# Optimization experiments

Hardware: AMD Instinct MI355X
Metric: run time of the kernel (lower is better)

The kernel has to match this reference:

```python
import jax, jax.numpy as jnp
import numpy as np

DIM = 1024
NUM_HEADS = 16
HEAD_DIM = DIM // NUM_HEADS


def apply_rotary_embed(x, thetas):
    # x: (..., seq, d), thetas: (seq, d) broadcast over leading dims
    x1, x2 = jnp.split(x, 2, axis=-1)
    x_rot = jnp.concatenate([-x2, x1], axis=-1)
    return x * jnp.cos(thetas) + x_rot * jnp.sin(thetas)


def setup_inputs() -> dict:
    key = jax.random.key(0)
    ks = jax.random.split(key, 8)
    B, Nx, Nc = 4, 1024, 2048
    x = jax.random.normal(ks[0], (B, Nx, DIM), dtype=jnp.float32)
    c = jax.random.normal(ks[1], (B, Nc, DIM), dtype=jnp.float32)
    x_pos_embed = jax.random.normal(ks[2], (Nx, HEAD_DIM), dtype=jnp.float32)
    c_pos_embed = jax.random.normal(ks[3], (Nc, HEAD_DIM), dtype=jnp.float32)
    s = 1.0 / np.sqrt(DIM)
    Wq = jax.random.normal(ks[4], (DIM, DIM), dtype=jnp.float32) * s
    Wkv = jax.random.normal(ks[5], (DIM, 2 * DIM), dtype=jnp.float32) * s
    Wproj = jax.random.normal(ks[6], (DIM, DIM), dtype=jnp.float32) * s
    bproj = jnp.zeros((DIM,), dtype=jnp.float32)
    return {"x": x, "c": c, "x_pos_embed": x_pos_embed, "c_pos_embed": c_pos_embed,
            "Wq": Wq, "Wkv": Wkv, "Wproj": Wproj, "bproj": bproj}


def reference(x, c, x_pos_embed, c_pos_embed, Wq, Wkv, Wproj, bproj):
    B, Nx, D = x.shape
    Nc = c.shape[1]
    H, hd = NUM_HEADS, HEAD_DIM
    # Q projection -> (B, H, Nx, hd)
    q = (x @ Wq).reshape(B, Nx, H, hd).transpose(0, 2, 1, 3)
    q = apply_rotary_embed(q, x_pos_embed)
    # KV projection -> k, v each (B, H, Nc, hd)
    kv = (c @ Wkv).reshape(B, Nc, 2, H, hd).transpose(2, 0, 3, 1, 4)
    k, v = kv[0], kv[1]
    k = apply_rotary_embed(k, c_pos_embed)
    # scaled dot-product attention (dropout p=0 -> identity)
    scale = 1.0 / np.sqrt(hd).astype(np.float32)
    attn = jnp.einsum('bhqd,bhkd->bhqk', q, k) * scale
    attn = jax.nn.softmax(attn, axis=-1)
    out = jnp.einsum('bhqk,bhkd->bhqd', attn, v)
    out = out.transpose(0, 2, 1, 3).reshape(B, Nx, D)
    return out @ Wproj + bproj
```

## Files before the change

kernel.cpp:

```cpp
#include <hip/hip_runtime.h>
#include <math.h>

#define DIMC  1024
#define NHEAD 16
#define HD    64
#define NB    4
#define NX    1024
#define NC    2048
#define KD    1024

typedef _Float16 half_t;
typedef __attribute__((ext_vector_type(8))) _Float16 h8;
typedef __attribute__((ext_vector_type(4))) _Float16 h4;
typedef __attribute__((ext_vector_type(4))) float f32x4;

#define QSCALE 0.1803368801111244f
#define NEGM  -8.656170245333781f

__device__ __forceinline__ void gload_lds16(const half_t* g, half_t* l) {
    __builtin_amdgcn_global_load_lds(
        (__attribute__((address_space(1))) void*)(g),
        (__attribute__((address_space(3))) void*)(l), 16, 0, 0);
}

__device__ __forceinline__ void wtile(const float* __restrict__ W,
                                      half_t* __restrict__ Wt, int N,
                                      int bx, int by, int t)
{
    __shared__ half_t T[64][72];
    const int k0 = by * 64, n0 = bx * 64;
    const int kr = t >> 2, c0 = (t & 3) << 4;
    const float* src = W + (size_t)(k0 + kr) * N + n0 + c0;
#pragma unroll
    for (int j = 0; j < 16; j += 4) {
        float4 v = *(const float4*)(src + j);
        T[c0 + j + 0][kr] = (half_t)v.x;
        T[c0 + j + 1][kr] = (half_t)v.y;
        T[c0 + j + 2][kr] = (half_t)v.z;
        T[c0 + j + 3][kr] = (half_t)v.w;
    }
    __syncthreads();
    const int nr = t >> 2, kc = (t & 3) << 4;
    half_t* dst = Wt + (size_t)(n0 + nr) * KD + k0 + kc;
    *(int4*)dst       = *(const int4*)&T[nr][kc];
    *(int4*)(dst + 8) = *(const int4*)&T[nr][kc + 8];
}

__global__ __launch_bounds__(256) void prep(
    const float* __restrict__ x, half_t* __restrict__ xh,
    const float* __restrict__ c, half_t* __restrict__ ch,
    const float* __restrict__ xpe, const float* __restrict__ cpe,
    float* __restrict__ xct, float* __restrict__ xst,
    float* __restrict__ cct, float* __restrict__ cst,
    const float* __restrict__ Wq,  half_t* __restrict__ Wqt,
    const float* __restrict__ Wkv, half_t* __restrict__ Wkt,
    const float* __restrict__ Wp,  half_t* __restrict__ Wpt)
{
    const int bid = blockIdx.x, t = threadIdx.x;
    if (bid < 1024) {
        if (bid < 256)      wtile(Wq,  Wqt, DIMC,     bid & 15,         bid >> 4,         t);
        else if (bid < 768) wtile(Wkv, Wkt, 2 * DIMC, (bid - 256) & 31, (bid - 256) >> 5, t);
        else                wtile(Wp,  Wpt, DIMC,     (bid - 768) & 15, (bid - 768) >> 4, t);
    } else if (bid < 7168) {
        const int nx = NB * NX * DIMC;
        const int i = ((bid - 1024) * 256 + t) * 8;
        const float* s;
        half_t* d;
        if (i < nx) { s = x + i; d = xh + i; }
        else        { s = c + (i - nx); d = ch + (i - nx); }
        float4 a = *(const float4*)(s);
        float4 b = *(const float4*)(s + 4);
        h8 o;
        o[0] = (half_t)a.x; o[1] = (half_t)a.y; o[2] = (half_t)a.z; o[3] = (half_t)a.w;
        o[4] = (half_t)b.x; o[5] = (half_t)b.y; o[6] = (half_t)b.z; o[7] = (half_t)b.w;
        *(h8*)d = o;
    } else {
        const int i = (bid - 7168) * 256 + t;
        if (i < NX * HD) {
            const float th = xpe[i];
            xct[i] = cosf(th); xst[i] = sinf(th);
        } else {
            const int j = i - NX * HD;
            const float th = cpe[j];
            cct[j] = cosf(th); cst[j] = sinf(th);
        }
    }
}

template <int MODE, int BN>
__global__ __launch_bounds__(256) void hgemm(
    const half_t* __restrict__ Ag, const half_t* __restrict__ Bt,
    const float* __restrict__ ct, const float* __restrict__ st,
    const float* __restrict__ bias,
    void* __restrict__ out0, void* __restrict__ out1)
{
    constexpr int MI = (BN == 128) ? 4 : 2;
    constexpr int BLOADS = BN / 32;
    __shared__ half_t As[8192];
    __shared__ half_t Bs[BN * 64];

    const int tid = threadIdx.x;
    const int w = tid >> 6, lane = tid & 63;
    const int lr = lane & 15, lg = lane >> 4;
    const int wrOff = (BN == 128) ? (w >> 1) * 64 : w * 32;
    const int wcOff = (BN == 128) ? (w & 1) * 64 : 0;

    int lin = (int)blockIdx.x;
    lin = (lin & 7) * ((int)gridDim.x >> 3) + (lin >> 3);
    const int m0 = (lin >> 4) * 128, n0 = (lin & 15) * BN;

    f32x4 acc[MI][4];
#pragma unroll
    for (int i = 0; i < MI; ++i)
#pragma unroll
        for (int j = 0; j < 4; ++j) acc[i][j] = f32x4{0.f, 0.f, 0.f, 0.f};

    size_t gA[4], gB[BLOADS];
    int loff[4];
#pragma unroll
    for (int c = 0; c < 4; ++c) {
        const int L = c * 4096 + w * 1024 + lane * 16;
        const int row = L >> 7;
        const int ss = ((L >> 4) & 7) ^ (row & 7);
        gA[c] = (size_t)(m0 + row) * KD + ss * 8;
        if (c < BLOADS) gB[c] = (size_t)(n0 + row) * KD + ss * 8;
        loff[c] = c * 2048 + w * 512;
    }

    for (int k0 = 0; k0 < KD; k0 += 64) {
#pragma unroll
        for (int c = 0; c < 4; ++c) {
            gload_lds16(Ag + gA[c] + k0, As + loff[c]);
            if (c < BLOADS) gload_lds16(Bt + gB[c] + k0, Bs + loff[c]);
        }
        __syncthreads();
#pragma unroll
        for (int kc = 0; kc < 2; ++kc) {
            h8 af[MI], bf[4];
#pragma unroll
            for (int mi = 0; mi < MI; ++mi) {
                const int r = wrOff + mi * 16 + lr;
                af[mi] = *(const h8*)&As[r * 64 + (((kc * 4 + lg) ^ (r & 7)) << 3)];
            }
#pragma unroll
            for (int ni = 0; ni < 4; ++ni) {
                const int r = wcOff + ni * 16 + lr;
                bf[ni] = *(const h8*)&Bs[r * 64 + (((kc * 4 + lg) ^ (r & 7)) << 3)];
            }
#pragma unroll
            for (int mi = 0; mi < MI; ++mi)
#pragma unroll
                for (int ni = 0; ni < 4; ++ni)
                    acc[mi][ni] = __builtin_amdgcn_mfma_f32_16x16x32_f16(
                        af[mi], bf[ni], acc[mi][ni], 0, 0, 0);
        }
        __syncthreads();
    }

    if (MODE == 2) {
        float* o = (float*)out0;
#pragma unroll
        for (int ni = 0; ni < 4; ++ni) {
            const int col = n0 + ni * 16 + lr;
            const float bv = bias[col];
#pragma unroll
            for (int mi = 0; mi < MI; ++mi)
#pragma unroll
                for (int r = 0; r < 4; ++r) {
                    const int row = m0 + wrOff + mi * 16 + lg * 4 + r;
                    o[(size_t)row * DIMC + col] = acc[mi][ni][r] + bv;
                }
        }
        return;
    }

    if (MODE == 0) {
        half_t* Qw = (half_t*)out0;
        const int h = n0 >> 6;
#pragma unroll
        for (int mi = 0; mi < MI; ++mi)
#pragma unroll
            for (int r = 0; r < 4; ++r) {
                const int row = m0 + wrOff + mi * 16 + lg * 4 + r;
                const int bb = row >> 10, nn = row & (NX - 1);
                const float* cr = ct + nn * HD;
                const float* sr = st + nn * HD;
                half_t* op = Qw + (((size_t)(bb * NHEAD + h)) * NX + nn) * HD;
#pragma unroll
                for (int ni = 0; ni < 4; ++ni) {
                    const int d = ni * 16 + lr;
                    const float val = acc[mi][ni][r];
                    const float pv  = acc[mi][ni ^ 2][r];
                    op[d] = (half_t)((val * cr[d] + (ni < 2 ? -pv : pv) * sr[d]) * QSCALE);
                }
            }
    } else {
        const bool isK = (n0 < DIMC);
        const int h = ((n0 & (DIMC - 1)) >> 6) + (w & 1);
        half_t* Kw = (half_t*)out0;
        half_t* Vw = (half_t*)out1;
#pragma unroll
        for (int mi = 0; mi < MI; ++mi)
#pragma unroll
            for (int r = 0; r < 4; ++r) {
                const int row = m0 + wrOff + mi * 16 + lg * 4 + r;
                const int bb = row >> 11, nn = row & (NC - 1);
                const int tt = nn >> 6, rr = nn & 63;
                const size_t tbase = ((size_t)(bb * NHEAD + h) * 32 + tt) * 4096;
                const float* cr = ct + nn * HD;
                const float* sr = st + nn * HD;
#pragma unroll
                for (int ni = 0; ni < 4; ++ni) {
                    const int d = ni * 16 + lr;
                    const float val = acc[mi][ni][r];
                    if (isK) {
                        const float pv = acc[mi][ni ^ 2][r];
                        Kw[tbase + rr * 64 + ((((d >> 3) ^ (rr & 7)) << 3) | (d & 7))] =
                            (half_t)(val * cr[d] + (ni < 2 ? -pv : pv) * sr[d]);
                    } else {
                        Vw[tbase + d * 64 + ((((rr >> 3) ^ (d & 7)) << 3) | (rr & 7))] =
                            (half_t)val;
                    }
                }
            }
    }
}

__global__ __launch_bounds__(256) void attn_mfma(
    const half_t* __restrict__ Q, const half_t* __restrict__ Kg,
    const half_t* __restrict__ Vg, half_t* __restrict__ O)
{
    __shared__ half_t Ks[2][4096];
    __shared__ half_t Vs[2][4096];
    __shared__ half_t Ps[4096];

    const int tid = threadIdx.x;
    const int w = tid >> 6, lane = tid & 63;
    const int lr = lane & 15, lg = lane >> 4;
    const int e7 = lr & 7;

    const int sid = (blockIdx.x & 7) * 128 + (blockIdx.x >> 3);
    const int bh = sid >> 4;
    const int q0 = (sid & 15) * 64;
    const int b = bh >> 4, h = bh & 15;

    const half_t* qbase = Q + ((size_t)bh * NX + q0 + w * 16 + lr) * HD + lg * 8;
    const h8 qf0 = *(const h8*)(qbase);
    const h8 qf1 = *(const h8*)(qbase + 32);

    f32x4 acc[4];
#pragma unroll
    for (int i = 0; i < 4; ++i) acc[i] = f32x4{0.f, 0.f, 0.f, 0.f};
    float lsum = 0.f;

    const half_t* Kt = Kg + (size_t)bh * 32 * 4096;
    const half_t* Vt = Vg + (size_t)bh * 32 * 4096;
    const int so = w * 512 + lane * 8;

#define STAGE(bi, t) do {                                           \
        const half_t* kg_ = Kt + (size_t)(t) * 4096;                \
        const half_t* vg_ = Vt + (size_t)(t) * 4096;                \
        gload_lds16(kg_ + so,        &Ks[bi][w * 512]);             \
        gload_lds16(kg_ + 2048 + so, &Ks[bi][2048 + w * 512]);      \
        gload_lds16(vg_ + so,        &Vs[bi][w * 512]);             \
        gload_lds16(vg_ + 2048 + so, &Vs[bi][2048 + w * 512]);      \
    } while (0)

    STAGE(0, 0);
    __syncthreads();

    const int rowq = w * 16 + lr;

    for (int t = 0; t < NC / 64; ++t) {
        const int cur = t & 1;
        if (t + 1 < NC / 64) STAGE(cur ^ 1, t + 1);

        f32x4 sc[4];
        __builtin_amdgcn_s_setprio(1);
#pragma unroll
        for (int cb = 0; cb < 4; ++cb) {
            const int r = cb * 16 + lr;
            const h8 kf0 = *(const h8*)&Ks[cur][r * 64 + ((lg ^ e7) << 3)];
            const h8 kf1 = *(const h8*)&Ks[cur][r * 64 + (((4 + lg) ^ e7) << 3)];
            f32x4 a = {NEGM, NEGM, NEGM, NEGM};
            a = __builtin_amdgcn_mfma_f32_16x16x32_f16(kf0, qf0, a, 0, 0, 0);
            a = __builtin_amdgcn_mfma_f32_16x16x32_f16(kf1, qf1, a, 0, 0, 0);
            sc[cb] = a;
        }
        __builtin_amdgcn_s_setprio(0);

        float p[4][4];
        float ps = 0.f;
#pragma unroll
        for (int cb = 0; cb < 4; ++cb)
#pragma unroll
            for (int r = 0; r < 4; ++r) {
                p[cb][r] = exp2f(sc[cb][r]);
                ps += p[cb][r];
            }
        ps += __shfl_xor(ps, 16);
        ps += __shfl_xor(ps, 32);
        lsum += ps;

#pragma unroll
        for (int cb = 0; cb < 4; ++cb) {
            h4 pk;
            pk[0] = (half_t)p[cb][0]; pk[1] = (half_t)p[cb][1];
            pk[2] = (half_t)p[cb][2]; pk[3] = (half_t)p[cb][3];
            const int s = cb * 2 + (lg >> 1);
            *(h4*)&Ps[rowq * 64 + ((s ^ e7) << 3) + (lg & 1) * 4] = pk;
        }

        const h8 pf0 = *(const h8*)&Ps[rowq * 64 + ((lg ^ e7) << 3)];
        const h8 pf1 = *(const h8*)&Ps[rowq * 64 + (((4 + lg) ^ e7) << 3)];
        __builtin_amdgcn_s_setprio(1);
#pragma unroll
        for (int db = 0; db < 4; ++db) {
            const int rd = db * 16 + lr;
            const h8 vf0 = *(const h8*)&Vs[cur][rd * 64 + ((lg ^ e7) << 3)];
            const h8 vf1 = *(const h8*)&Vs[cur][rd * 64 + (((4 + lg) ^ e7) << 3)];
            acc[db] = __builtin_amdgcn_mfma_f32_16x16x32_f16(pf0, vf0, acc[db], 0, 0, 0);
            acc[db] = __builtin_amdgcn_mfma_f32_16x16x32_f16(pf1, vf1, acc[db], 0, 0, 0);
        }
        __builtin_amdgcn_s_setprio(0);

        __syncthreads();
    }
#undef STAGE

    const float inv = 1.f / lsum;
    float invs[4];
#pragma unroll
    for (int r = 0; r < 4; ++r) invs[r] = __shfl(inv, lg * 4 + r);

    half_t* Ob = O + ((size_t)b * NX + q0 + w * 16) * DIMC + h * HD;
#pragma unroll
    for (int db = 0; db < 4; ++db)
#pragma unroll
        for (int r = 0; r < 4; ++r)
            Ob[(size_t)(lg * 4 + r) * DIMC + db * 16 + lr] =
                (half_t)(acc[db][r] * invs[r]);
}

extern "C" void kernel_launch(void* const* d_in, const int* in_sizes, int n_in,
                              void* d_out, int out_size, void* d_ws, size_t ws_size,
                              hipStream_t stream)
{
    const float* x     = (const float*)d_in[0];
    const float* c     = (const float*)d_in[1];
    const float* xpe   = (const float*)d_in[2];
    const float* cpe   = (const float*)d_in[3];
    const float* Wq    = (const float*)d_in[4];
    const float* Wkv   = (const float*)d_in[5];
    const float* Wproj = (const float*)d_in[6];
    const float* bproj = (const float*)d_in[7];

    char* wsb = (char*)d_ws;
    half_t* xh  = (half_t*)(wsb);
    half_t* ch  = (half_t*)(wsb + ((size_t)8  << 20));
    half_t* Wqt = (half_t*)(wsb + ((size_t)24 << 20));
    half_t* Wkt = (half_t*)(wsb + ((size_t)26 << 20));
    half_t* Wpt = (half_t*)(wsb + ((size_t)30 << 20));
    half_t* Kw  = (half_t*)(wsb + ((size_t)32 << 20));
    half_t* Vw  = (half_t*)(wsb + ((size_t)48 << 20));
    half_t* Ow  = (half_t*)(wsb + ((size_t)64 << 20));
    float*  xct = (float*)(wsb + ((size_t)72 << 20));
    float*  xst = (float*)(wsb + ((size_t)72 << 20) + (256u << 10));
    float*  cct = (float*)(wsb + ((size_t)72 << 20) + (512u << 10));
    float*  cst = (float*)(wsb + ((size_t)72 << 20) + (1024u << 10));
    half_t* Qw  = (half_t*)d_out;

    prep<<<7936, 256, 0, stream>>>(x, xh, c, ch, xpe, cpe,
                                   xct, xst, cct, cst,
                                   Wq, Wqt, Wkv, Wkt, Wproj, Wpt);

    hgemm<0, 64><<<512, 256, 0, stream>>>(xh, Wqt, xct, xst, nullptr,
                                          Qw, nullptr);
    hgemm<1, 128><<<1024, 256, 0, stream>>>(ch, Wkt, cct, cst, nullptr,
                                            Kw, Vw);
    attn_mfma<<<1024, 256, 0, stream>>>(Qw, Kw, Vw, Ow);
    hgemm<2, 64><<<512, 256, 0, stream>>>(Ow, Wpt, nullptr, nullptr, bproj,
                                          (float*)d_out, nullptr);
}
```

Measured before the change: 193.2 us.

## Double-buffer GEMM LDS loads and compute softmax row sums via MFMA

The GEMM main loop moves to two LDS buffers: the next K tile is prefetched while the current one is consumed, with explicit vmcnt waits and raw barriers in place of __syncthreads. The attention kernel uses the same explicit wait and barrier scheme. It also drops the per-tile shuffle reduction for the softmax denominator and instead accumulates row sums with an extra MFMA against a ones vector, converting exp values using packed RTZ conversion. The goal is to overlap global loads with MFMA work and cut VALU and shuffle overhead. The cost is doubled LDS use in the GEMM, which may lower occupancy. The vmcnt constants are hand-tuned and fragile, and the row sums are now taken from fp16-rounded probabilities.

Result: faster. 188.8 us (-2.2%).

```diff
diff --git a/kernel.cpp b/kernel.cpp
--- a/kernel.cpp
+++ b/kernel.cpp
@@ -12,6 +12,7 @@
 typedef _Float16 half_t;
 typedef __attribute__((ext_vector_type(8))) _Float16 h8;
 typedef __attribute__((ext_vector_type(4))) _Float16 h4;
+typedef __attribute__((ext_vector_type(2))) __fp16 fp16x2;
 typedef __attribute__((ext_vector_type(4))) float f32x4;
 
 #define QSCALE 0.1803368801111244f
@@ -96,8 +97,8 @@
 {
     constexpr int MI = (BN == 128) ? 4 : 2;
     constexpr int BLOADS = BN / 32;
-    __shared__ half_t As[8192];
-    __shared__ half_t Bs[BN * 64];
+    __shared__ half_t As[2][8192];
+    __shared__ half_t Bs[2][BN * 64];
 
     const int tid = threadIdx.x;
     const int w = tid >> 6, lane = tid & 63;
@@ -127,25 +128,46 @@
         loff[c] = c * 2048 + w * 512;
     }
 
-    for (int k0 = 0; k0 < KD; k0 += 64) {
-#pragma unroll
-        for (int c = 0; c < 4; ++c) {
-            gload_lds16(Ag + gA[c] + k0, As + loff[c]);
-            if (c < BLOADS) gload_lds16(Bt + gB[c] + k0, Bs + loff[c]);
-        }
-        __syncthreads();
+#define HSTAGE(buf, kk) do {                                               \
+        _Pragma("unroll")                                                  \
+        for (int c = 0; c < 4; ++c) {                                      \
+            gload_lds16(Ag + gA[c] + (kk) * 64, &As[buf][loff[c]]);        \
+            if (c < BLOADS) gload_lds16(Bt + gB[c] + (kk) * 64, &Bs[buf][loff[c]]); \
+        }                                                                  \
+    } while (0)
+
+    HSTAGE(0, 0);
+    asm volatile("s_waitcnt vmcnt(0)" ::: "memory");
+    __builtin_amdgcn_s_barrier();
+    __builtin_amdgcn_sched_barrier(0);
+
+    for (int k = 0; k < KD / 64; ++k) {
+        const int cb = k & 1;
+        if (k + 1 < KD / 64) {
+            HSTAGE(cb ^ 1, k + 1);
+            if constexpr (BLOADS == 4)
+                asm volatile("s_waitcnt vmcnt(8)" ::: "memory");
+            else
+                asm volatile("s_waitcnt vmcnt(6)" ::: "memory");
+        } else {
+            asm volatile("s_waitcnt vmcnt(0)" ::: "memory");
+        }
+        __builtin_amdgcn_s_barrier();
+        __builtin_amdgcn_sched_barrier(0);
+
+        __builtin_amdgcn_s_setprio(1);
 #pragma unroll
         for (int kc = 0; kc < 2; ++kc) {
             h8 af[MI], bf[4];
 #pragma unroll
             for (int mi = 0; mi < MI; ++mi) {
                 const int r = wrOff + mi * 16 + lr;
-                af[mi] = *(const h8*)&As[r * 64 + (((kc * 4 + lg) ^ (r & 7)) << 3)];
+                af[mi] = *(const h8*)&As[cb][r * 64 + (((kc * 4 + lg) ^ (r & 7)) << 3)];
             }
 #pragma unroll
             for (int ni = 0; ni < 4; ++ni) {
                 const int r = wcOff + ni * 16 + lr;
-                bf[ni] = *(const h8*)&Bs[r * 64 + (((kc * 4 + lg) ^ (r & 7)) << 3)];
+                bf[ni] = *(const h8*)&Bs[cb][r * 64 + (((kc * 4 + lg) ^ (r & 7)) << 3)];
             }
 #pragma unroll
             for (int mi = 0; mi < MI; ++mi)
@@ -154,8 +176,12 @@
                     acc[mi][ni] = __builtin_amdgcn_mfma_f32_16x16x32_f16(
                         af[mi], bf[ni], acc[mi][ni], 0, 0, 0);
         }
-        __syncthreads();
-    }
+        __builtin_amdgcn_s_setprio(0);
+
+        __builtin_amdgcn_s_barrier();
+        __builtin_amdgcn_sched_barrier(0);
+    }
+#undef HSTAGE
 
     if (MODE == 2) {
         float* o = (float*)out0;
@@ -251,7 +277,11 @@
     f32x4 acc[4];
 #pragma unroll
     for (int i = 0; i < 4; ++i) acc[i] = f32x4{0.f, 0.f, 0.f, 0.f};
-    float lsum = 0.f;
+    f32x4 accl = {0.f, 0.f, 0.f, 0.f};
+
+    h8 vone;
+#pragma unroll
+    for (int i = 0; i < 8; ++i) vone[i] = (half_t)(lr == 0 ? 1.0f : 0.0f);
 
     const half_t* Kt = Kg + (size_t)bh * 32 * 4096;
     const half_t* Vt = Vg + (size_t)bh * 32 * 4096;
@@ -267,13 +297,22 @@
     } while (0)
 
     STAGE(0, 0);
-    __syncthreads();
+    asm volatile("s_waitcnt vmcnt(0)" ::: "memory");
+    __builtin_amdgcn_s_barrier();
+    __builtin_amdgcn_sched_barrier(0);
 
     const int rowq = w * 16 + lr;
 
     for (int t = 0; t < NC / 64; ++t) {
         const int cur = t & 1;
-        if (t + 1 < NC / 64) STAGE(cur ^ 1, t + 1);
+        if (t + 1 < NC / 64) {
+            STAGE(cur ^ 1, t + 1);
+            asm volatile("s_waitcnt vmcnt(8)" ::: "memory");
+        } else {
+            asm volatile("s_waitcnt vmcnt(0)" ::: "memory");
+        }
+        __builtin_amdgcn_s_barrier();
+        __builtin_amdgcn_sched_barrier(0);
 
         f32x4 sc[4];
         __builtin_amdgcn_s_setprio(1);
@@ -289,26 +328,15 @@
         }
         __builtin_amdgcn_s_setprio(0);
 
-        float p[4][4];
-        float ps = 0.f;
-#pragma unroll
-        for (int cb = 0; cb < 4; ++cb)
-#pragma unroll
-            for (int r = 0; r < 4; ++r) {
-                p[cb][r] = exp2f(sc[cb][r]);
-                ps += p[cb][r];
-            }
-        ps += __shfl_xor(ps, 16);
-        ps += __shfl_xor(ps, 32);
-        lsum += ps;
-
 #pragma unroll
         for (int cb = 0; cb < 4; ++cb) {
-            h4 pk;
-            pk[0] = (half_t)p[cb][0]; pk[1] = (half_t)p[cb][1];
-            pk[2] = (half_t)p[cb][2]; pk[3] = (half_t)p[cb][3];
+            fp16x2 a01 = __builtin_amdgcn_cvt_pkrtz(exp2f(sc[cb][0]), exp2f(sc[cb][1]));
+            fp16x2 a23 = __builtin_amdgcn_cvt_pkrtz(exp2f(sc[cb][2]), exp2f(sc[cb][3]));
+            union { h4 h; uint2 u; } pw;
+            pw.u.x = *(unsigned int*)&a01;
+            pw.u.y = *(unsigned int*)&a23;
             const int s = cb * 2 + (lg >> 1);
-            *(h4*)&Ps[rowq * 64 + ((s ^ e7) << 3) + (lg & 1) * 4] = pk;
+            *(h4*)&Ps[rowq * 64 + ((s ^ e7) << 3) + (lg & 1) * 4] = pw.h;
         }
 
         const h8 pf0 = *(const h8*)&Ps[rowq * 64 + ((lg ^ e7) << 3)];
@@ -322,16 +350,19 @@
             acc[db] = __builtin_amdgcn_mfma_f32_16x16x32_f16(pf0, vf0, acc[db], 0, 0, 0);
             acc[db] = __builtin_amdgcn_mfma_f32_16x16x32_f16(pf1, vf1, acc[db], 0, 0, 0);
         }
+        accl = __builtin_amdgcn_mfma_f32_16x16x32_f16(pf0, vone, accl, 0, 0, 0);
+        accl = __builtin_amdgcn_mfma_f32_16x16x32_f16(pf1, vone, accl, 0, 0, 0);
         __builtin_amdgcn_s_setprio(0);
 
-        __syncthreads();
+        __builtin_amdgcn_s_barrier();
+        __builtin_amdgcn_sched_barrier(0);
     }
 #undef STAGE
 
-    const float inv = 1.f / lsum;
     float invs[4];
 #pragma unroll
-    for (int r = 0; r < 4; ++r) invs[r] = __shfl(inv, lg * 4 + r);
+    for (int r = 0; r < 4; ++r)
+        invs[r] = 1.f / __shfl(accl[r], lg << 4);
 
     half_t* Ob = O + ((size_t)b * NX + q0 + w * 16) * DIMC + h * HD;
 #pragma unroll
```
